# Kernel optimization log

Measured on AMD Instinct MI355X. Metric: run time of the kernel, lower is better.

## Reference

```python
import jax, jax.numpy as jnp
import numpy as np

WINDOW_SIZE = 11
SIGMA = 1.5
C1 = 0.01 ** 2
C2 = 0.03 ** 2


def _gaussian_window_3d(window_size=WINDOW_SIZE, sigma=SIGMA):
    # 1D gaussian, normalized, then separable outer product -> dense 3D kernel
    x = jnp.arange(window_size, dtype=jnp.float32)
    g = jnp.exp(-((x - window_size // 2) ** 2) / (2.0 * sigma ** 2))
    g = g / g.sum()
    w3 = g[:, None, None] * g[None, :, None] * g[None, None, :]  # [ws,ws,ws]
    return w3[None, None]  # [O=1, I=1, D, H, W]


def _conv3d_same(x, w):
    # x: [N,1,D,H,W], w: [1,1,ws,ws,ws]; 'SAME' padding matches torch padding=ws//2 for odd ws
    return jax.lax.conv_general_dilated(
        x, w, window_strides=(1, 1, 1), padding='SAME',
        dimension_numbers=('NCDHW', 'OIDHW', 'NCDHW'))


def setup_inputs() -> dict:
    key = jax.random.key(0)
    k1, k2 = jax.random.split(key)
    shape = (4, 1, 160, 160, 160)
    img1 = jax.random.uniform(k1, shape, dtype=jnp.float32)
    img2 = jax.random.uniform(k2, shape, dtype=jnp.float32)
    return {"img1": img1, "img2": img2}


def reference(img1, img2):
    window = _gaussian_window_3d()
    mu1 = _conv3d_same(img1, window)
    mu2 = _conv3d_same(img2, window)
    mu1_sq = mu1 * mu1
    mu2_sq = mu2 * mu2
    mu1_mu2 = mu1 * mu2
    sigma1_sq = _conv3d_same(img1 * img1, window) - mu1_sq
    sigma2_sq = _conv3d_same(img2 * img2, window) - mu2_sq
    sigma12 = _conv3d_same(img1 * img2, window) - mu1_mu2
    ssim_map = ((2.0 * mu1_mu2 + C1) * (2.0 * sigma12 + C2)) / (
        (mu1_sq + mu2_sq + C1) * (sigma1_sq + sigma2_sq + C2))
    return 1.0 - ssim_map.mean()
```

## Files before the change

### kernel.cpp

```cpp
#include <hip/hip_runtime.h>
#include <hip/hip_bf16.h>
#include <math.h>

#define WW     160
#define NBATCH 4
#define VOL    (160*160*160)
#define PLANE  (160*160)

#define C1f 0.0001f
#define C2f 0.0009f

#define RUN_H 16
#define NROWS (RUN_H + 10)
#define LDW2  172
#define RUN_D 20
#define ITERS (RUN_D + 10)
#define PF    8

typedef float v2f __attribute__((ext_vector_type(2)));

struct Gw { float g[11]; };

__device__ __forceinline__ float bf2f(unsigned short u) {
    return __uint_as_float(((unsigned int)u) << 16);
}
__device__ __forceinline__ unsigned short f2bf(float f) {
    __hip_bfloat16 h = __float2bfloat16(f);
    return *reinterpret_cast<unsigned short*>(&h);
}

__global__ __launch_bounds__(192, 3) void k_wh(
    const float* __restrict__ x, const float* __restrict__ y,
    ushort4* __restrict__ B4, Gw gw)
{
    __shared__ v2f tile[NROWS][LDW2];
    const int t  = threadIdx.x;
    const int h0 = blockIdx.x * RUN_H;
    const int d  = blockIdx.y;
    const int n  = blockIdx.z;

    const float* xb = x + (size_t)n * VOL + (size_t)d * PLANE;
    const float* yb = y + (size_t)n * VOL + (size_t)d * PLANE;

#pragma unroll 4
    for (int s = t; s < NROWS * LDW2; s += 192) {
        int r = s / LDW2, c = s - r * LDW2;
        int h = h0 - 5 + r;
        int w = c - 5;
        v2f v = {0.f, 0.f};
        if (h >= 0 && h < 160 && w >= 0 && w < 160) {
            size_t idx = (size_t)h * WW + w;
            v.x = xb[idx];
            v.y = yb[idx];
        }
        tile[r][c] = v;
    }
    __syncthreads();

    if (t < 160) {
        const int w = t;
        const size_t outbase = (size_t)n * VOL + (size_t)d * PLANE + w;
        v2f   r01[11];
        float rs[11];
        float r4[11];

#define WSTEP(i) { \
        v2f a01 = {0.f, 0.f}, a23 = {0.f, 0.f}; float a4 = 0.f; \
        _Pragma("unroll") \
        for (int k = 0; k < 5; ++k) { \
            v2f p1 = tile[i][w + k]; \
            v2f p2 = tile[i][w + 10 - k]; \
            float g = gw.g[k]; v2f g2 = {g, g}; \
            a01 += g2 * (p1 + p2); \
            v2f sq = p1 * p1; \
            sq += p2 * p2; \
            a23 += g2 * sq; \
            float pr = p1.x * p1.y; \
            pr = fmaf(p2.x, p2.y, pr); \
            a4 = fmaf(g, pr, a4); \
        } \
        { \
            v2f p = tile[i][w + 5]; \
            float g = gw.g[5]; v2f g2 = {g, g}; \
            a01 += g2 * p; \
            a23 += g2 * (p * p); \
            a4  = fmaf(g, p.x * p.y, a4); \
        } \
        r01[(i) % 11] = a01; \
        rs [(i) % 11] = a23.x + a23.y; \
        r4 [(i) % 11] = a4; \
        if ((i) >= 10) { \
            const int j = (i) - 10; \
            v2f o01 = {0.f, 0.f}; float os = 0.f, o4 = 0.f; \
            _Pragma("unroll") \
            for (int k = 0; k < 11; ++k) { \
                float g = gw.g[k]; v2f g2 = {g, g}; \
                o01 += g2 * r01[(j + k) % 11]; \
                os = fmaf(g, rs[(j + k) % 11], os); \
                o4 = fmaf(g, r4[(j + k) % 11], o4); \
            } \
            size_t oi = outbase + (size_t)(h0 + j) * WW; \
            ushort4 u4; \
            u4.x = f2bf(o01.x); \
            u4.y = f2bf(o01.y); \
            u4.z = f2bf(os); \
            u4.w = f2bf(o4); \
            B4[oi] = u4; \
        } }

        WSTEP(0)  WSTEP(1)  WSTEP(2)  WSTEP(3)  WSTEP(4)  WSTEP(5)
        WSTEP(6)  WSTEP(7)  WSTEP(8)  WSTEP(9)  WSTEP(10) WSTEP(11)
        WSTEP(12) WSTEP(13) WSTEP(14) WSTEP(15) WSTEP(16) WSTEP(17)
        WSTEP(18) WSTEP(19) WSTEP(20) WSTEP(21) WSTEP(22) WSTEP(23)
        WSTEP(24) WSTEP(25)
#undef WSTEP
    }
}

__global__ __launch_bounds__(256, 3) void k_dssim(
    const ushort4* __restrict__ B4, double* __restrict__ accum, Gw gw)
{
    const int tid = threadIdx.x;
    const int p   = blockIdx.x * 256 + tid;
    const int d0  = blockIdx.y * RUN_D;
    const int n   = blockIdx.z;
    const size_t base = (size_t)n * VOL + p;

    v2f ring01[11], ring23[11];
    float lsum = 0.f;

    ushort4 pf[PF];
    {
        const bool front_ok = (d0 != 0);
#pragma unroll
        for (int q = 0; q < PF; ++q) {
            bool ok = (q >= 5) || front_ok;
            pf[q] = make_ushort4(0, 0, 0, 0);
            if (ok) {
                size_t idx = base + (size_t)(d0 - 5 + q) * PLANE;
                pf[q] = B4[idx];
            }
        }
    }

#pragma unroll
    for (int i = 0; i < ITERS; ++i) {
        ushort4 c4 = pf[i % PF];
        ring01[i%11] = (v2f){ bf2f(c4.x), bf2f(c4.y) };
        ring23[i%11] = (v2f){ bf2f(c4.z), bf2f(c4.w) };

        if (i + PF < ITERS) {
            const int dd = d0 + i + 3;
            const bool ok = (dd < 160);
            pf[i % PF] = make_ushort4(0, 0, 0, 0);
            if (ok) {
                size_t idx = base + (size_t)dd * PLANE;
                pf[i % PF] = B4[idx];
            }
        }

        if (i >= 10) {
            const int j = i - 10;
            v2f o01 = {0.f, 0.f}, o23 = {0.f, 0.f};
#pragma unroll
            for (int k = 0; k < 11; ++k) {
                float g = gw.g[k];
                v2f g2 = {g, g};
                o01 += g2 * ring01[(j + k) % 11];
                o23 += g2 * ring23[(j + k) % 11];
            }
            float mu1 = o01.x, mu2 = o01.y;
            float s   = o23.x, e12 = o23.y;
            float m11  = mu1 * mu2;
            float musq = fmaf(mu1, mu1, mu2 * mu2);
            float num = (2.f * m11 + C1f) * (2.f * (e12 - m11) + C2f);
            float den = (musq + C1f) * ((s - musq) + C2f);
            lsum += num * __builtin_amdgcn_rcpf(den);
        }
    }

    __shared__ float wsum[4];
    const int lane = tid & 63, wi = tid >> 6;
#pragma unroll
    for (int off = 32; off > 0; off >>= 1)
        lsum += __shfl_down(lsum, off, 64);
    if (lane == 0) wsum[wi] = lsum;
    __syncthreads();
    if (tid == 0)
        atomicAdd(accum, (double)(wsum[0] + wsum[1] + wsum[2] + wsum[3]));
}

__global__ void k_final(const double* __restrict__ accum, float* __restrict__ out)
{
    out[0] = (float)(1.0 - accum[0] / ((double)NBATCH * (double)VOL));
}

extern "C" void kernel_launch(void* const* d_in, const int* in_sizes, int n_in,
                              void* d_out, int out_size, void* d_ws, size_t ws_size,
                              hipStream_t stream)
{
    const float* img1 = (const float*)d_in[0];
    const float* img2 = (const float*)d_in[1];
    float* out = (float*)d_out;

    char* ws = (char*)d_ws;
    ushort4* B4 = (ushort4*)ws;
    double* accum = (double*)(ws + (size_t)NBATCH * VOL * 8);

    Gw gw;
    {
        double gd[11], s = 0.0;
        for (int i = 0; i < 11; ++i) {
            double t = (double)(i - 5);
            gd[i] = exp(-(t * t) / (2.0 * 1.5 * 1.5));
            s += gd[i];
        }
        for (int i = 0; i < 11; ++i) gw.g[i] = (float)(gd[i] / s);
    }

    hipMemsetAsync(accum, 0, sizeof(double), stream);

    k_wh   <<<dim3(160 / RUN_H, 160, NBATCH), 192, 0, stream>>>(img1, img2, B4, gw);
    k_dssim<<<dim3(PLANE / 256, 160 / RUN_D, NBATCH), 256, 0, stream>>>(B4, accum, gw);
    k_final<<<1, 1, 0, stream>>>(accum, out);
}
```

Before: 320.7 us.

## Pack shared tile as bf16 pairs, lengthen depth runs, raise occupancy bounds

The first-pass shared tile now stores each x/y pair as two packed bf16 values in one 32-bit word instead of two floats. This halves LDS footprint and read bandwidth and allows higher occupancy via launch_bounds 4. The vertical-stage register rings are merged into packed float2 so the H-convolution can use packed FMAs. The depth run per thread doubles, cutting the halo reload overhead in the D pass. The risks are extra precision loss from rounding inputs to bf16 before the convolutions, and more register pressure under the tighter occupancy bound.

```diff
diff --git a/kernel.cpp b/kernel.cpp
--- a/kernel.cpp
+++ b/kernel.cpp
@@ -12,8 +12,8 @@
 
 #define RUN_H 16
 #define NROWS (RUN_H + 10)
-#define LDW2  172
-#define RUN_D 20
+#define LDW   176
+#define RUN_D 40
 #define ITERS (RUN_D + 10)
 #define PF    8
 
@@ -29,11 +29,11 @@
     return *reinterpret_cast<unsigned short*>(&h);
 }
 
-__global__ __launch_bounds__(192, 3) void k_wh(
+__global__ __launch_bounds__(192, 4) void k_wh(
     const float* __restrict__ x, const float* __restrict__ y,
     ushort4* __restrict__ B4, Gw gw)
 {
-    __shared__ v2f tile[NROWS][LDW2];
+    __shared__ unsigned int tile[NROWS][LDW];
     const int t  = threadIdx.x;
     const int h0 = blockIdx.x * RUN_H;
     const int d  = blockIdx.y;
@@ -43,33 +43,34 @@
     const float* yb = y + (size_t)n * VOL + (size_t)d * PLANE;
 
 #pragma unroll 4
-    for (int s = t; s < NROWS * LDW2; s += 192) {
-        int r = s / LDW2, c = s - r * LDW2;
+    for (int s = t; s < NROWS * LDW; s += 192) {
+        int r = s / LDW, c = s - r * LDW;
         int h = h0 - 5 + r;
         int w = c - 5;
-        v2f v = {0.f, 0.f};
+        float vx = 0.f, vy = 0.f;
         if (h >= 0 && h < 160 && w >= 0 && w < 160) {
             size_t idx = (size_t)h * WW + w;
-            v.x = xb[idx];
-            v.y = yb[idx];
-        }
-        tile[r][c] = v;
+            vx = xb[idx];
+            vy = yb[idx];
+        }
+        tile[r][c] = ((unsigned int)f2bf(vy) << 16) | (unsigned int)f2bf(vx);
     }
     __syncthreads();
 
     if (t < 160) {
         const int w = t;
         const size_t outbase = (size_t)n * VOL + (size_t)d * PLANE + w;
-        v2f   r01[11];
-        float rs[11];
-        float r4[11];
+        v2f r01[11];
+        v2f r23[11];
 
 #define WSTEP(i) { \
         v2f a01 = {0.f, 0.f}, a23 = {0.f, 0.f}; float a4 = 0.f; \
         _Pragma("unroll") \
         for (int k = 0; k < 5; ++k) { \
-            v2f p1 = tile[i][w + k]; \
-            v2f p2 = tile[i][w + 10 - k]; \
+            unsigned int u1 = tile[i][w + k]; \
+            unsigned int u2 = tile[i][w + 10 - k]; \
+            v2f p1 = { __uint_as_float(u1 << 16), __uint_as_float(u1 & 0xffff0000u) }; \
+            v2f p2 = { __uint_as_float(u2 << 16), __uint_as_float(u2 & 0xffff0000u) }; \
             float g = gw.g[k]; v2f g2 = {g, g}; \
             a01 += g2 * (p1 + p2); \
             v2f sq = p1 * p1; \
@@ -80,31 +81,30 @@
             a4 = fmaf(g, pr, a4); \
         } \
         { \
-            v2f p = tile[i][w + 5]; \
+            unsigned int u = tile[i][w + 5]; \
+            v2f p = { __uint_as_float(u << 16), __uint_as_float(u & 0xffff0000u) }; \
             float g = gw.g[5]; v2f g2 = {g, g}; \
             a01 += g2 * p; \
             a23 += g2 * (p * p); \
             a4  = fmaf(g, p.x * p.y, a4); \
         } \
         r01[(i) % 11] = a01; \
-        rs [(i) % 11] = a23.x + a23.y; \
-        r4 [(i) % 11] = a4; \
+        r23[(i) % 11] = (v2f){ a23.x + a23.y, a4 }; \
         if ((i) >= 10) { \
             const int j = (i) - 10; \
-            v2f o01 = {0.f, 0.f}; float os = 0.f, o4 = 0.f; \
+            v2f o01 = {0.f, 0.f}, o23 = {0.f, 0.f}; \
             _Pragma("unroll") \
             for (int k = 0; k < 11; ++k) { \
                 float g = gw.g[k]; v2f g2 = {g, g}; \
                 o01 += g2 * r01[(j + k) % 11]; \
-                os = fmaf(g, rs[(j + k) % 11], os); \
-                o4 = fmaf(g, r4[(j + k) % 11], o4); \
+                o23 += g2 * r23[(j + k) % 11]; \
             } \
             size_t oi = outbase + (size_t)(h0 + j) * WW; \
             ushort4 u4; \
             u4.x = f2bf(o01.x); \
             u4.y = f2bf(o01.y); \
-            u4.z = f2bf(os); \
-            u4.w = f2bf(o4); \
+            u4.z = f2bf(o23.x); \
+            u4.w = f2bf(o23.y); \
             B4[oi] = u4; \
         } }
 
@@ -117,7 +117,7 @@
     }
 }
 
-__global__ __launch_bounds__(256, 3) void k_dssim(
+__global__ __launch_bounds__(256, 4) void k_dssim(
     const ushort4* __restrict__ B4, double* __restrict__ accum, Gw gw)
 {
     const int tid = threadIdx.x;
```

Result: faster. 274.6 us (-14.4%).
